# Kernel tuning notes

Measured on AMD Instinct MI355X. Metric: run time of the kernel, lower is better.

Reference implementation:

```python
import jax, jax.numpy as jnp
from jax import lax
import numpy as np

L, B, E, D, V, MID = 128, 32, 512, 1024, 32000, 4


def sru_layer(x, c0, W, b, use_tanh=True):
    """One SRU layer. x: (L,B,n_in), c0: (B,n_out), W: (n_in, k*n_out), b: (2*n_out)."""
    n_out = c0.shape[-1]
    k = W.shape[1] // n_out
    U = jnp.einsum('lbi,io->lbo', x, W)  # parallel GEMM over all timesteps
    x_tilde = U[..., :n_out]
    f = jax.nn.sigmoid(U[..., n_out:2 * n_out] + b[:n_out])
    r = jax.nn.sigmoid(U[..., 2 * n_out:3 * n_out] + b[n_out:])
    hw = U[..., 3 * n_out:] if k == 4 else x  # highway path

    def step(c, fx):
        f_t, xt_t = fx
        c = f_t * c + (1.0 - f_t) * xt_t
        return c, c

    c_last, cs = lax.scan(step, c0, (f, x_tilde))
    g = jnp.tanh(cs) if use_tanh else cs
    h = r * g + (1.0 - r) * hw
    return h, c_last


def setup_inputs() -> dict:
    key = jax.random.key(0)
    ks = jax.random.split(key, 8)
    s_e = (3.0 / E) ** 0.5
    s_d = (3.0 / D) ** 0.5
    return {
        'x': jax.random.randint(ks[0], (L, B), 0, V, dtype=jnp.int64),
        'c1': jnp.zeros((B, D), jnp.float32),
        'c2': jnp.zeros((MID, B, D), jnp.float32),
        'c3': jnp.zeros((B, E), jnp.float32),
        'emb': jax.random.uniform(ks[1], (V, E), jnp.float32, -s_d, s_d),
        'out_bias': jnp.zeros((V,), jnp.float32),
        'W1': jax.random.uniform(ks[2], (E, 4 * D), jnp.float32, -s_e, s_e),
        'b1': jnp.zeros((2 * D,), jnp.float32),
        'W2': jax.random.uniform(ks[3], (MID, D, 3 * D), jnp.float32, -s_d, s_d),
        'b2': jnp.zeros((MID, 2 * D), jnp.float32),
        'W3': jax.random.uniform(ks[4], (D, 4 * E), jnp.float32, -s_d, s_d),
        'b3': jnp.zeros((2 * E,), jnp.float32),
    }


def reference(x, c1, c2, c3, emb, out_bias, W1, b1, W2, b2, W3, b3):
    h = emb[x]  # (L,B,E) embedding lookup (dropout=0 in eval)
    h, _ = sru_layer(h, c1, W1, b1)            # E -> D (k=4)
    for i in range(W2.shape[0]):               # D -> D stacked (k=3)
        h, _ = sru_layer(h, c2[i], W2[i], b2[i])
    h, _ = sru_layer(h, c3, W3, b3)            # D -> E (k=4)
    logits = h.reshape(-1, E) @ emb.T + out_bias  # tied-weight projection (L*B, V)
    return logits
```

## Files before the change

kernel.cpp:

```cpp
#include <hip/hip_runtime.h>


typedef __attribute__((ext_vector_type(8))) __bf16 bf16x8;
typedef __attribute__((ext_vector_type(4))) float f32x4;
typedef __attribute__((ext_vector_type(4))) float float4v;
typedef __attribute__((ext_vector_type(4))) unsigned short u16x4;

__device__ __forceinline__ unsigned short f2bf(float f) {
  unsigned int u = __builtin_bit_cast(unsigned int, f);
  u += 0x7fffu + ((u >> 16) & 1u);
  return (unsigned short)(u >> 16);
}
__device__ __forceinline__ float bf2f(unsigned short v) {
  unsigned int u = ((unsigned int)v) << 16;
  return __builtin_bit_cast(float, u);
}

#define GLDS16(SRC, DST)                                                      \
  __builtin_amdgcn_global_load_lds(                                           \
      (__attribute__((address_space(1))) void*)(SRC),                         \
      (__attribute__((address_space(3))) void*)(DST), 16, 0, 0)

template <bool BF16OUT, bool GATHER>
__global__ __launch_bounds__(256, 4)
void gemm128(const unsigned short* __restrict__ A,
             const unsigned short* __restrict__ B,
             void* __restrict__ Cv, const float* __restrict__ bias,
             const int* __restrict__ xrow,
             int M, int N, int K, int tiles_m) {
  __shared__ __align__(16) unsigned short As[128 * 64];
  __shared__ __align__(16) unsigned short Bs[128 * 64];
  __shared__ int xs[128];

  const int tid  = threadIdx.x;
  const int lane = tid & 63;
  const int wave = tid >> 6;
  const int wm = wave >> 1, wn = wave & 1;

  const int nwg  = gridDim.x;
  const int orig = blockIdx.x;
  const int wg   = (orig & 7) * (nwg >> 3) + (orig >> 3);
  const int by = wg % tiles_m, bx = wg / tiles_m;
  const int m0 = by * 128, n0 = bx * 128;

  if constexpr (GATHER) {
    if (tid < 128) xs[tid] = xrow[m0 + tid];
    __syncthreads();
  }

  const int srow  = lane >> 3;
  const int sslot = (lane & 7) ^ srow;
  const int fr = lane & 15;
  const int s0 = (lane >> 4) ^ (lane & 7);
  const int lg = lane >> 4;

  f32x4 acc[4][4] = {};

  const int ksteps = K >> 6;
  for (int ks = 0; ks < ksteps; ++ks) {
    const int k0 = ks << 6;
#pragma unroll
    for (int j = 0; j < 4; ++j) {
      const int rbase = (j * 4 + wave) * 8;
      const int r = rbase + srow;
      const unsigned short* sa;
      if constexpr (GATHER)
        sa = A + (size_t)xs[r] * K + k0 + sslot * 8;
      else
        sa = A + (size_t)(m0 + r) * K + k0 + sslot * 8;
      const unsigned short* sb = B + (size_t)(n0 + r) * K + k0 + sslot * 8;
      GLDS16(sa, &As[rbase * 64]);
      GLDS16(sb, &Bs[rbase * 64]);
    }
    __syncthreads();
#pragma unroll
    for (int kk = 0; kk < 2; ++kk) {
      const int slot = s0 ^ (kk << 2);
      bf16x8 a[4], b[4];
#pragma unroll
      for (int m = 0; m < 4; ++m)
        a[m] = *(const bf16x8*)&As[(wm * 64 + m * 16 + fr) * 64 + slot * 8];
#pragma unroll
      for (int n = 0; n < 4; ++n)
        b[n] = *(const bf16x8*)&Bs[(wn * 64 + n * 16 + fr) * 64 + slot * 8];
#pragma unroll
      for (int m = 0; m < 4; ++m)
#pragma unroll
        for (int n = 0; n < 4; ++n)
          acc[m][n] = __builtin_amdgcn_mfma_f32_16x16x32_bf16(a[m], b[n],
                                                              acc[m][n], 0, 0, 0);
    }
    __syncthreads();
  }

  if constexpr (BF16OUT) {
    unsigned short* C = (unsigned short*)Cv;
#pragma unroll
    for (int m = 0; m < 4; ++m) {
      const int row = m0 + wm * 64 + m * 16 + lg * 4;
#pragma unroll
      for (int r = 0; r < 4; ++r) {
        unsigned short* Crow = C + (size_t)(row + r) * N + n0 + wn * 64 + fr;
#pragma unroll
        for (int n = 0; n < 4; ++n)
          Crow[n * 16] = f2bf(acc[m][n][r]);
      }
    }
  } else {
    float* C = (float*)Cv;
    float bv[4];
#pragma unroll
    for (int n = 0; n < 4; ++n)
      bv[n] = bias ? bias[n0 + wn * 64 + n * 16 + fr] : 0.0f;
#pragma unroll
    for (int m = 0; m < 4; ++m) {
      const int row = m0 + wm * 64 + m * 16 + lg * 4;
#pragma unroll
      for (int r = 0; r < 4; ++r) {
        float* Crow = C + (size_t)(row + r) * N + n0 + wn * 64 + fr;
#pragma unroll
        for (int n = 0; n < 4; ++n)
          __builtin_nontemporal_store(acc[m][n][r] + bv[n], &Crow[n * 16]);
      }
    }
  }
}

template <bool K4>
__global__ __launch_bounds__(256)
void scan_k(const unsigned short* __restrict__ U,
            const float* __restrict__ bias,
            const float* __restrict__ c0v,
            const unsigned short* __restrict__ hin,
            unsigned short* __restrict__ hout, int n_out) {
  __shared__ float lA[4][64], lB[4][64];
  const int lane = threadIdx.x & 63;
  const int ch   = threadIdx.x >> 6;
  const int idx  = blockIdx.x * 64 + lane;
  const int b = idx / n_out;
  const int d = idx - b * n_out;
  const float biasf = bias[d];
  const float biasr = bias[n_out + d];
  const int rowlen = (K4 ? 4 : 3) * n_out;
  const size_t lstride = (size_t)32 * rowlen;
  const size_t hstride = (size_t)32 * n_out;
  const unsigned short* Up0 = U + (size_t)b * rowlen + d + (size_t)(ch * 32) * lstride;

  float A = 1.0f, Bv = 0.0f;
  {
    const unsigned short* p = Up0;
    float xt0, fr0, xt1, fr1, xt2, fr2, xt3, fr3;
#define P1_LOAD(S)                                                            \
    do { xt##S = bf2f(p[0]); fr##S = bf2f(p[n_out]); p += lstride; } while (0)
#define P1_STEP(S)                                                            \
    do {                                                                      \
      const float f = 1.0f / (1.0f + __expf(-(fr##S + biasf)));               \
      A *= f;  Bv = f * Bv + (1.0f - f) * xt##S;                              \
    } while (0)
    P1_LOAD(0); P1_LOAD(1); P1_LOAD(2); P1_LOAD(3);
    for (int s = 0; s < 28; s += 4) {
      P1_STEP(0); P1_LOAD(0);
      P1_STEP(1); P1_LOAD(1);
      P1_STEP(2); P1_LOAD(2);
      P1_STEP(3); P1_LOAD(3);
    }
    P1_STEP(0); P1_STEP(1); P1_STEP(2); P1_STEP(3);
#undef P1_LOAD
#undef P1_STEP
  }
  lA[ch][lane] = A;
  lB[ch][lane] = Bv;
  __syncthreads();

  float c = c0v[idx];
  for (int i = 0; i < ch; ++i)
    c = lA[i][lane] * c + lB[i][lane];

  {
    const unsigned short* p = Up0;
    const unsigned short* hp = hin + (size_t)b * n_out + d + (size_t)(ch * 32) * hstride;
    unsigned short* op = hout + (size_t)b * n_out + d + (size_t)(ch * 32) * hstride;
    float xt0, fr0, rr0, hw0, xt1, fr1, rr1, hw1;
    float xt2, fr2, rr2, hw2, xt3, fr3, rr3, hw3;
#define P2_LOAD(S)                                                            \
    do {                                                                      \
      xt##S = bf2f(p[0]);                                                     \
      fr##S = bf2f(p[n_out]);                                                 \
      rr##S = bf2f(p[2 * n_out]);                                             \
      hw##S = K4 ? bf2f(p[3 * n_out]) : bf2f(*hp);                            \
      p += lstride;                                                           \
      hp += hstride;                                                          \
    } while (0)
#define P2_STEP(S)                                                            \
    do {                                                                      \
      const float f = 1.0f / (1.0f + __expf(-(fr##S + biasf)));               \
      const float r = 1.0f / (1.0f + __expf(-(rr##S + biasr)));               \
      c = f * c + (1.0f - f) * xt##S;                                         \
      const float e2 = __expf(2.0f * c);                                      \
      const float g = 1.0f - 2.0f / (e2 + 1.0f);                              \
      *op = f2bf(r * g + (1.0f - r) * hw##S);                                 \
      op += hstride;                                                          \
    } while (0)
    P2_LOAD(0); P2_LOAD(1); P2_LOAD(2); P2_LOAD(3);
    for (int s = 0; s < 28; s += 4) {
      P2_STEP(0); P2_LOAD(0);
      P2_STEP(1); P2_LOAD(1);
      P2_STEP(2); P2_LOAD(2);
      P2_STEP(3); P2_LOAD(3);
    }
    P2_STEP(0); P2_STEP(1); P2_STEP(2); P2_STEP(3);
#undef P2_LOAD
#undef P2_STEP
  }
}

__device__ __forceinline__ void transpose_tile64(const float* __restrict__ W,
                                                 unsigned short* __restrict__ Wt,
                                                 int K, int N, int bx, int by,
                                                 int tid) {
  __shared__ float tile[64][65];
  const int n0 = bx * 64, k0 = by * 64;
  const int tx = tid & 63, ty = tid >> 6;
#pragma unroll
  for (int i = 0; i < 64; i += 4)
    tile[ty + i][tx] = W[(size_t)(k0 + ty + i) * N + n0 + tx];
  __syncthreads();
#pragma unroll
  for (int i = 0; i < 64; i += 4)
    Wt[(size_t)(n0 + ty + i) * K + k0 + tx] = f2bf(tile[tx][ty + i]);
}

__global__ void prep_k(const float* __restrict__ emb,
                       const float* __restrict__ W1,
                       const float* __restrict__ W2,
                       const float* __restrict__ W3,
                       unsigned short* __restrict__ embbf,
                       unsigned short* __restrict__ W1t,
                       unsigned short* __restrict__ W2t,
                       unsigned short* __restrict__ W3t) {
  const int blk = blockIdx.x;
  const int tid = threadIdx.x;
  if (blk < 16000) {
    const int i = blk * 256 + tid;
    const float4v v = ((const float4v*)emb)[i];
    u16x4 o;
    o.x = f2bf(v.x); o.y = f2bf(v.y); o.z = f2bf(v.z); o.w = f2bf(v.w);
    ((u16x4*)embbf)[i] = o;
  } else if (blk < 16512) {
    const int r = blk - 16000;
    transpose_tile64(W1, W1t, 512, 4096, r & 63, r >> 6, tid);
  } else if (blk < 19584) {
    const int r = blk - 16512;
    const int i = r / 768, rr = r - i * 768;
    transpose_tile64(W2 + (size_t)i * 3145728, W2t + (size_t)i * 3145728,
                     1024, 3072, rr % 48, rr / 48, tid);
  } else {
    const int r = blk - 19584;
    transpose_tile64(W3, W3t, 1024, 2048, r & 31, r >> 5, tid);
  }
}

extern "C" void kernel_launch(void* const* d_in, const int* in_sizes, int n_in,
                              void* d_out, int out_size, void* d_ws, size_t ws_size,
                              hipStream_t stream) {
  (void)in_sizes; (void)n_in; (void)out_size; (void)ws_size;
  const int*   x     = (const int*)d_in[0];
  const float* c1    = (const float*)d_in[1];
  const float* c2    = (const float*)d_in[2];
  const float* c3    = (const float*)d_in[3];
  const float* emb   = (const float*)d_in[4];
  const float* obias = (const float*)d_in[5];
  const float* W1    = (const float*)d_in[6];
  const float* b1    = (const float*)d_in[7];
  const float* W2    = (const float*)d_in[8];
  const float* b2    = (const float*)d_in[9];
  const float* W3    = (const float*)d_in[10];
  const float* b3    = (const float*)d_in[11];

  char* ws = (char*)d_ws;
  unsigned short* hbfA  = (unsigned short*)ws;
  unsigned short* hbfB  = (unsigned short*)(ws + 8388608);
  unsigned short* embbf = (unsigned short*)(ws + 16777216);
  unsigned short* W1t   = (unsigned short*)(ws + 49545216);
  unsigned short* W2t   = (unsigned short*)(ws + 53739520);
  unsigned short* W3t   = (unsigned short*)(ws + 78905344);
  unsigned short* U = (unsigned short*)d_out;

  prep_k<<<20096, 256, 0, stream>>>(emb, W1, W2, W3, embbf, W1t, W2t, W3t);

  gemm128<true, true><<<1024, 256, 0, stream>>>(embbf, W1t, U, nullptr, x,
                                                4096, 4096, 512, 32);
  scan_k<true><<<512, 256, 0, stream>>>(U, b1, c1, hbfB, hbfB, 1024);

  const unsigned short* hin = hbfB;
  unsigned short* hout = hbfA;
  for (int i = 0; i < 4; ++i) {
    gemm128<true, false><<<768, 256, 0, stream>>>(hin, W2t + (size_t)i * 3145728,
                                                  U, nullptr, nullptr,
                                                  4096, 3072, 1024, 32);
    scan_k<false><<<512, 256, 0, stream>>>(U, b2 + i * 2048, c2 + (size_t)i * 32768,
                                           hin, hout, 1024);
    const unsigned short* t = hin; hin = hout; hout = (unsigned short*)t;
  }

  gemm128<true, false><<<512, 256, 0, stream>>>(hin, W3t, U, nullptr, nullptr,
                                                4096, 2048, 1024, 32);
  scan_k<true><<<256, 256, 0, stream>>>(U, b3, c3, hout, hout, 512);

  gemm128<false, false><<<8000, 256, 0, stream>>>(hout, embbf, (float*)d_out,
                                                  obias, nullptr,
                                                  4096, 32000, 512, 32);
}
```

Measured before the change: 463.3 us.

## Split scan into 8 time chunks and cache forget gates between passes

The chunked SRU scan now uses 8 chunks of 16 timesteps per block (512 threads) instead of 4 chunks of 32. This shortens each thread's serial recurrence and raises the number of waves in flight. The forget gate and the weighted input from the first pass are kept in registers, so the second pass no longer reloads x_tilde and f or recomputes the sigmoid. The cost is more registers per thread and a longer serial prefix combine across chunks.

```diff
diff --git a/kernel.cpp b/kernel.cpp
--- a/kernel.cpp
+++ b/kernel.cpp
@@ -127,13 +127,13 @@
 }
 
 template <bool K4>
-__global__ __launch_bounds__(256)
+__global__ __launch_bounds__(512)
 void scan_k(const unsigned short* __restrict__ U,
             const float* __restrict__ bias,
             const float* __restrict__ c0v,
             const unsigned short* __restrict__ hin,
             unsigned short* __restrict__ hout, int n_out) {
-  __shared__ float lA[4][64], lB[4][64];
+  __shared__ float lA[8][64], lB[8][64];
   const int lane = threadIdx.x & 63;
   const int ch   = threadIdx.x >> 6;
   const int idx  = blockIdx.x * 64 + lane;
@@ -144,29 +144,23 @@
   const int rowlen = (K4 ? 4 : 3) * n_out;
   const size_t lstride = (size_t)32 * rowlen;
   const size_t hstride = (size_t)32 * n_out;
-  const unsigned short* Up0 = U + (size_t)b * rowlen + d + (size_t)(ch * 32) * lstride;
-
+  const unsigned short* Up0 = U + (size_t)b * rowlen + d + (size_t)(ch * 16) * lstride;
+
+  float fv[16], wv[16];
   float A = 1.0f, Bv = 0.0f;
   {
     const unsigned short* p = Up0;
-    float xt0, fr0, xt1, fr1, xt2, fr2, xt3, fr3;
-#define P1_LOAD(S)                                                            \
-    do { xt##S = bf2f(p[0]); fr##S = bf2f(p[n_out]); p += lstride; } while (0)
-#define P1_STEP(S)                                                            \
-    do {                                                                      \
-      const float f = 1.0f / (1.0f + __expf(-(fr##S + biasf)));               \
-      A *= f;  Bv = f * Bv + (1.0f - f) * xt##S;                              \
-    } while (0)
-    P1_LOAD(0); P1_LOAD(1); P1_LOAD(2); P1_LOAD(3);
-    for (int s = 0; s < 28; s += 4) {
-      P1_STEP(0); P1_LOAD(0);
-      P1_STEP(1); P1_LOAD(1);
-      P1_STEP(2); P1_LOAD(2);
-      P1_STEP(3); P1_LOAD(3);
-    }
-    P1_STEP(0); P1_STEP(1); P1_STEP(2); P1_STEP(3);
-#undef P1_LOAD
-#undef P1_STEP
+#pragma unroll
+    for (int s = 0; s < 16; ++s) {
+      const float xt   = bf2f(p[0]);
+      const float fraw = bf2f(p[n_out]);
+      p += lstride;
+      const float f = 1.0f / (1.0f + __expf(-(fraw + biasf)));
+      fv[s] = f;
+      wv[s] = (1.0f - f) * xt;
+      A *= f;
+      Bv = f * Bv + wv[s];
+    }
   }
   lA[ch][lane] = A;
   lB[ch][lane] = Bv;
@@ -178,39 +172,21 @@
 
   {
     const unsigned short* p = Up0;
-    const unsigned short* hp = hin + (size_t)b * n_out + d + (size_t)(ch * 32) * hstride;
-    unsigned short* op = hout + (size_t)b * n_out + d + (size_t)(ch * 32) * hstride;
-    float xt0, fr0, rr0, hw0, xt1, fr1, rr1, hw1;
-    float xt2, fr2, rr2, hw2, xt3, fr3, rr3, hw3;
-#define P2_LOAD(S)                                                            \
-    do {                                                                      \
-      xt##S = bf2f(p[0]);                                                     \
-      fr##S = bf2f(p[n_out]);                                                 \
-      rr##S = bf2f(p[2 * n_out]);                                             \
-      hw##S = K4 ? bf2f(p[3 * n_out]) : bf2f(*hp);                            \
-      p += lstride;                                                           \
-      hp += hstride;                                                          \
-    } while (0)
-#define P2_STEP(S)                                                            \
-    do {                                                                      \
-      const float f = 1.0f / (1.0f + __expf(-(fr##S + biasf)));               \
-      const float r = 1.0f / (1.0f + __expf(-(rr##S + biasr)));               \
-      c = f * c + (1.0f - f) * xt##S;                                         \
-      const float e2 = __expf(2.0f * c);                                      \
-      const float g = 1.0f - 2.0f / (e2 + 1.0f);                              \
-      *op = f2bf(r * g + (1.0f - r) * hw##S);                                 \
-      op += hstride;                                                          \
-    } while (0)
-    P2_LOAD(0); P2_LOAD(1); P2_LOAD(2); P2_LOAD(3);
-    for (int s = 0; s < 28; s += 4) {
-      P2_STEP(0); P2_LOAD(0);
-      P2_STEP(1); P2_LOAD(1);
-      P2_STEP(2); P2_LOAD(2);
-      P2_STEP(3); P2_LOAD(3);
-    }
-    P2_STEP(0); P2_STEP(1); P2_STEP(2); P2_STEP(3);
-#undef P2_LOAD
-#undef P2_STEP
+    const unsigned short* hp = hin + (size_t)b * n_out + d + (size_t)(ch * 16) * hstride;
+    unsigned short* op = hout + (size_t)b * n_out + d + (size_t)(ch * 16) * hstride;
+#pragma unroll
+    for (int s = 0; s < 16; ++s) {
+      const float rr = bf2f(p[2 * n_out]);
+      const float hw = K4 ? bf2f(p[3 * n_out]) : bf2f(*hp);
+      p += lstride;
+      hp += hstride;
+      c = fv[s] * c + wv[s];
+      const float r = 1.0f / (1.0f + __expf(-(rr + biasr)));
+      const float e2 = __expf(2.0f * c);
+      const float g = 1.0f - 2.0f / (e2 + 1.0f);
+      *op = f2bf(r * g + (1.0f - r) * hw);
+      op += hstride;
+    }
   }
 }
 
@@ -290,7 +266,7 @@
 
   gemm128<true, true><<<1024, 256, 0, stream>>>(embbf, W1t, U, nullptr, x,
                                                 4096, 4096, 512, 32);
-  scan_k<true><<<512, 256, 0, stream>>>(U, b1, c1, hbfB, hbfB, 1024);
+  scan_k<true><<<512, 512, 0, stream>>>(U, b1, c1, hbfB, hbfB, 1024);
 
   const unsigned short* hin = hbfB;
   unsigned short* hout = hbfA;
@@ -298,14 +274,14 @@
     gemm128<true, false><<<768, 256, 0, stream>>>(hin, W2t + (size_t)i * 3145728,
                                                   U, nullptr, nullptr,
                                                   4096, 3072, 1024, 32);
-    scan_k<false><<<512, 256, 0, stream>>>(U, b2 + i * 2048, c2 + (size_t)i * 32768,
+    scan_k<false><<<512, 512, 0, stream>>>(U, b2 + i * 2048, c2 + (size_t)i * 32768,
                                            hin, hout, 1024);
     const unsigned short* t = hin; hin = hout; hout = (unsigned short*)t;
   }
 
   gemm128<true, false><<<512, 256, 0, stream>>>(hin, W3t, U, nullptr, nullptr,
                                                 4096, 2048, 1024, 32);
-  scan_k<true><<<256, 256, 0, stream>>>(U, b3, c3, hout, hout, 512);
+  scan_k<true><<<256, 512, 0, stream>>>(U, b3, c3, hout, hout, 512);
 
   gemm128<false, false><<<8000, 256, 0, stream>>>(hout, embbf, (float*)d_out,
                                                   obias, nullptr,
```

After: 435.7 us. 6.0% less time.
